# Optimization experiments

Hardware: AMD Instinct MI355X
Metric: run time of the kernel (lower is better)

Reference implementation:

```python
import jax, jax.numpy as jnp
import numpy as np

N_NODES = 50000


def setup_inputs() -> dict:
    key = jax.random.key(0)
    k1, k2, k3, k4, k5 = jax.random.split(key, 5)
    h = jax.random.normal(k1, (50000, 256), dtype=jnp.float32)
    norm = jax.random.uniform(k2, (50000, 1), dtype=jnp.float32)
    weight = jax.random.normal(k3, (256, 96), dtype=jnp.float32) * (1.0 / np.sqrt(96.0))
    src = jax.random.randint(k4, (800000,), 0, N_NODES, dtype=jnp.int64)
    dst = jax.random.randint(k5, (800000,), 0, N_NODES, dtype=jnp.int64)
    return {"h": h, "norm": norm, "weight": weight, "src": src, "dst": dst}


def reference(h, norm, weight, src, dst):
    # dense projection: [N, in] @ [in, out] -> [N, out]
    hw = jnp.matmul(h, weight)
    # pre-aggregation degree norm
    hw = hw * norm
    # copy_src + sum: gather messages from src, scatter-add into dst
    msgs = hw[src]  # [E, out]
    agg = jax.ops.segment_sum(msgs, dst, num_segments=N_NODES)
    # post-aggregation degree norm + activation
    out = jax.nn.relu(agg * norm)
    return out
```

## Files before the change

kernel.cpp:

```cpp
#include <hip/hip_runtime.h>

#define M_NODES 50000
#define KDIM    256
#define NDIM    96
#define NEDGE   800000
#define BM      64
#define NPB     64
#define NBUCK   782
#define CAPB    1536
#define EPB     2048
#define NBLK_SC 391

typedef short bf16x8 __attribute__((ext_vector_type(8)));
typedef float f32x4  __attribute__((ext_vector_type(4)));

__device__ inline unsigned short f2bf(float x) {
    unsigned u = __float_as_uint(x);
    u = (u + 0x7fffu + ((u >> 16) & 1u)) >> 16;
    return (unsigned short)u;
}
__device__ inline unsigned pack2bf(float x, float y) {
    return (unsigned)f2bf(x) | ((unsigned)f2bf(y) << 16);
}

__global__ __launch_bounds__(256) void prep_w_kernel(
    const float* __restrict__ w, unsigned short* __restrict__ wt,
    int* __restrict__ gcursor)
{
    if (blockIdx.x == 0)
        for (int i = threadIdx.x; i < NBUCK; i += 256)
            gcursor[i] = i * CAPB;
    int i = blockIdx.x * 256 + threadIdx.x;
    if (i < KDIM * NDIM) {
        int n = i >> 8;
        int k = i & 255;
        wt[i] = f2bf(w[(size_t)k * NDIM + n]);
    }
}

__global__ __launch_bounds__(256) void gemm_mfma_kernel(
    const float* __restrict__ h, const float* __restrict__ norm,
    const unsigned short* __restrict__ wt, unsigned short* __restrict__ hwb)
{
    __shared__ unsigned short w_lds[96 * 256];

    const int tid  = threadIdx.x;
    const int lane = tid & 63;
    const int wv   = tid >> 6;
    const int row0 = blockIdx.x * BM;

#pragma unroll
    for (int it = 0; it < 12; ++it) {
        int idx = tid + it * 256;
        int n   = idx >> 5;
        int kb  = (idx & 31) * 16;
        uint4 v = *reinterpret_cast<const uint4*>(
            reinterpret_cast<const char*>(wt) + n * 512 + kb);
        *reinterpret_cast<uint4*>(
            reinterpret_cast<char*>(w_lds) + n * 512 + (kb ^ ((n & 7) << 4))) = v;
    }
    __syncthreads();

    f32x4 acc[6];
#pragma unroll
    for (int f = 0; f < 6; ++f) acc[f] = (f32x4){0.f, 0.f, 0.f, 0.f};

    const int ar  = wv * 16 + (lane & 15);
    const int kg  = lane >> 4;
    int arow = row0 + ar;
    if (arow >= M_NODES) arow = M_NODES - 1;
    const float* __restrict__ hrow = h + (size_t)arow * KDIM;

#pragma unroll
    for (int s = 0; s < 8; ++s) {
        const int k0 = s * 32 + kg * 8;
        float4 p = *reinterpret_cast<const float4*>(hrow + k0);
        float4 q = *reinterpret_cast<const float4*>(hrow + k0 + 4);
        union { bf16x8 v; unsigned u[4]; } a;
        a.u[0] = pack2bf(p.x, p.y);
        a.u[1] = pack2bf(p.z, p.w);
        a.u[2] = pack2bf(q.x, q.y);
        a.u[3] = pack2bf(q.z, q.w);

        const int kb = s * 64 + kg * 16;
#pragma unroll
        for (int f = 0; f < 6; ++f) {
            int n = f * 16 + (lane & 15);
            bf16x8 b = *reinterpret_cast<const bf16x8*>(
                reinterpret_cast<const char*>(w_lds) + n * 512 + (kb ^ ((n & 7) << 4)));
            acc[f] = __builtin_amdgcn_mfma_f32_16x16x32_bf16(a.v, b, acc[f], 0, 0, 0);
        }
    }

    const int crow = wv * 16 + (lane >> 4) * 4;
    const int ccol = lane & 15;
#pragma unroll
    for (int r = 0; r < 4; ++r) {
        int row = row0 + crow + r;
        if (row < M_NODES) {
            float nv = norm[row];
#pragma unroll
            for (int f = 0; f < 6; ++f)
                hwb[(size_t)row * NDIM + f * 16 + ccol] = f2bf(acc[f][r] * nv);
        }
    }
}

__global__ __launch_bounds__(256) void bin_scatter_kernel(
    const int* __restrict__ src, const int* __restrict__ dst,
    int* __restrict__ gcursor, unsigned* __restrict__ binned)
{
    __shared__ int cnt[NBUCK];
    __shared__ int base[NBUCK];
    const int t  = threadIdx.x;
    const int e0 = blockIdx.x * EPB;
    const int e1 = (e0 + EPB < NEDGE) ? e0 + EPB : NEDGE;

    for (int i = t; i < NBUCK; i += 256) cnt[i] = 0;
    __syncthreads();
    for (int e = e0 + t; e < e1; e += 256)
        atomicAdd(&cnt[dst[e] >> 6], 1);
    __syncthreads();
    for (int i = t; i < NBUCK; i += 256) {
        int c = cnt[i];
        base[i] = c ? atomicAdd(&gcursor[i], c) : 0;
    }
    __syncthreads();
    for (int i = t; i < NBUCK; i += 256) cnt[i] = 0;
    __syncthreads();
    for (int e = e0 + t; e < e1; e += 256) {
        int d = dst[e];
        int b = d >> 6;
        int pos = base[b] + atomicAdd(&cnt[b], 1);
        if (pos < (b + 1) * CAPB)
            binned[pos] = ((unsigned)(d & 63) << 16) | (unsigned)src[e];
    }
}

#define ACC8(v)                                        \
    acc[0] += __uint_as_float((v).x << 16);            \
    acc[1] += __uint_as_float((v).x & 0xffff0000u);    \
    acc[2] += __uint_as_float((v).y << 16);            \
    acc[3] += __uint_as_float((v).y & 0xffff0000u);    \
    acc[4] += __uint_as_float((v).z << 16);            \
    acc[5] += __uint_as_float((v).z & 0xffff0000u);    \
    acc[6] += __uint_as_float((v).w << 16);            \
    acc[7] += __uint_as_float((v).w & 0xffff0000u);

__global__ __launch_bounds__(256) void csr_agg_kernel(
    const unsigned* __restrict__ binned, const int* __restrict__ gcursor,
    const unsigned short* __restrict__ hwb, const float* __restrict__ norm,
    float* __restrict__ out)
{
    __shared__ unsigned eL[CAPB];
    __shared__ unsigned short oL[CAPB];
    __shared__ int cnt[NPB];
    __shared__ int pfxE[NPB];

    const int b  = blockIdx.x;
    const int t  = threadIdx.x;
    const int e0 = b * CAPB;
    int cntE = gcursor[b] - e0;
    if (cntE > CAPB) cntE = CAPB;

    for (int i = t; i < cntE; i += 256) eL[i] = binned[e0 + i];
    if (t < NPB) cnt[t] = 0;
    __syncthreads();
    for (int i = t; i < cntE; i += 256)
        atomicAdd(&cnt[(eL[i] >> 16) & 63], 1);
    __syncthreads();
    if (t < NPB) pfxE[t] = cnt[t];
    __syncthreads();
    for (int st = 1; st < NPB; st <<= 1) {
        int o = (t >= st && t < NPB) ? pfxE[t - st] : 0;
        __syncthreads();
        if (t < NPB) pfxE[t] += o;
        __syncthreads();
    }
    if (t < NPB) {
        int ex = pfxE[t] - cnt[t];
        pfxE[t] = ex;
        cnt[t]  = ex;
    }
    __syncthreads();
    for (int i = t; i < cntE; i += 256) {
        unsigned v = eL[i];
        int d = (v >> 16) & 63;
        int p = atomicAdd(&cnt[d], 1);
        oL[p] = (unsigned short)(v & 0xffffu);
    }
    __syncthreads();

#pragma unroll
    for (int pass = 0; pass < 3; ++pass) {
        const int u     = pass * 256 + t;
        const int node  = u / 12;
        const int c8    = u - node * 12;
        const int gnode = b * NPB + node;
        if (gnode < M_NODES) {
            const int s0 = pfxE[node];
            const int s1 = cnt[node];
            float acc[8] = {0.f, 0.f, 0.f, 0.f, 0.f, 0.f, 0.f, 0.f};
            int e = s0;
            for (; e + 2 <= s1; e += 2) {
                int a0 = oL[e], a1 = oL[e + 1];
                uint4 v0 = *reinterpret_cast<const uint4*>(hwb + (size_t)a0 * NDIM + c8 * 8);
                uint4 v1 = *reinterpret_cast<const uint4*>(hwb + (size_t)a1 * NDIM + c8 * 8);
                ACC8(v0); ACC8(v1);
            }
            if (e < s1) {
                int a0 = oL[e];
                uint4 v0 = *reinterpret_cast<const uint4*>(hwb + (size_t)a0 * NDIM + c8 * 8);
                ACC8(v0);
            }
            const float nv = norm[gnode];
            float4 o0, o1;
            o0.x = fmaxf(acc[0] * nv, 0.f); o0.y = fmaxf(acc[1] * nv, 0.f);
            o0.z = fmaxf(acc[2] * nv, 0.f); o0.w = fmaxf(acc[3] * nv, 0.f);
            o1.x = fmaxf(acc[4] * nv, 0.f); o1.y = fmaxf(acc[5] * nv, 0.f);
            o1.z = fmaxf(acc[6] * nv, 0.f); o1.w = fmaxf(acc[7] * nv, 0.f);
            float4* po = reinterpret_cast<float4*>(out + (size_t)gnode * NDIM + c8 * 8);
            po[0] = o0; po[1] = o1;
        }
    }
}

extern "C" void kernel_launch(void* const* d_in, const int* in_sizes, int n_in,
                              void* d_out, int out_size, void* d_ws, size_t ws_size,
                              hipStream_t stream)
{
    const float* h    = (const float*)d_in[0];
    const float* norm = (const float*)d_in[1];
    const float* w    = (const float*)d_in[2];
    const int*   src  = (const int*)d_in[3];
    const int*   dst  = (const int*)d_in[4];
    float* out = (float*)d_out;

    unsigned short* hwb = (unsigned short*)d_ws;
    unsigned short* wt  = hwb + (size_t)M_NODES * NDIM;
    int* gcursor = (int*)(wt + KDIM * NDIM);
    unsigned* binned = (unsigned*)(gcursor + 800);

    prep_w_kernel<<<(KDIM * NDIM + 255) / 256, 256, 0, stream>>>(w, wt, gcursor);
    bin_scatter_kernel<<<NBLK_SC, 256, 0, stream>>>(src, dst, gcursor, binned);
    gemm_mfma_kernel<<<(M_NODES + BM - 1) / BM, 256, 0, stream>>>(h, norm, wt, hwb);
    csr_agg_kernel<<<NBUCK, 256, 0, stream>>>(binned, gcursor, hwb, norm, out);
}
```

Measured before the change: 75.89 us.

## Merge GEMM and edge binning into one launch, double GEMM rows per block

```diff
diff --git a/kernel.cpp b/kernel.cpp
--- a/kernel.cpp
+++ b/kernel.cpp
@@ -4,7 +4,8 @@
 #define KDIM    256
 #define NDIM    96
 #define NEDGE   800000
-#define BM      64
+#define BM      128
+#define GEMM_BLKS 391
 #define NPB     64
 #define NBUCK   782
 #define CAPB    1536
@@ -38,114 +39,131 @@
     }
 }
 
-__global__ __launch_bounds__(256) void gemm_mfma_kernel(
+__global__ __launch_bounds__(256) void fused_gemm_scatter_kernel(
     const float* __restrict__ h, const float* __restrict__ norm,
-    const unsigned short* __restrict__ wt, unsigned short* __restrict__ hwb)
-{
-    __shared__ unsigned short w_lds[96 * 256];
-
-    const int tid  = threadIdx.x;
-    const int lane = tid & 63;
-    const int wv   = tid >> 6;
-    const int row0 = blockIdx.x * BM;
-
-#pragma unroll
-    for (int it = 0; it < 12; ++it) {
-        int idx = tid + it * 256;
-        int n   = idx >> 5;
-        int kb  = (idx & 31) * 16;
-        uint4 v = *reinterpret_cast<const uint4*>(
-            reinterpret_cast<const char*>(wt) + n * 512 + kb);
-        *reinterpret_cast<uint4*>(
-            reinterpret_cast<char*>(w_lds) + n * 512 + (kb ^ ((n & 7) << 4))) = v;
-    }
-    __syncthreads();
-
-    f32x4 acc[6];
-#pragma unroll
-    for (int f = 0; f < 6; ++f) acc[f] = (f32x4){0.f, 0.f, 0.f, 0.f};
-
-    const int ar  = wv * 16 + (lane & 15);
-    const int kg  = lane >> 4;
-    int arow = row0 + ar;
-    if (arow >= M_NODES) arow = M_NODES - 1;
-    const float* __restrict__ hrow = h + (size_t)arow * KDIM;
-
-#pragma unroll
-    for (int s = 0; s < 8; ++s) {
-        const int k0 = s * 32 + kg * 8;
-        float4 p = *reinterpret_cast<const float4*>(hrow + k0);
-        float4 q = *reinterpret_cast<const float4*>(hrow + k0 + 4);
-        union { bf16x8 v; unsigned u[4]; } a;
-        a.u[0] = pack2bf(p.x, p.y);
-        a.u[1] = pack2bf(p.z, p.w);
-        a.u[2] = pack2bf(q.x, q.y);
-        a.u[3] = pack2bf(q.z, q.w);
-
-        const int kb = s * 64 + kg * 16;
-#pragma unroll
-        for (int f = 0; f < 6; ++f) {
-            int n = f * 16 + (lane & 15);
-            bf16x8 b = *reinterpret_cast<const bf16x8*>(
-                reinterpret_cast<const char*>(w_lds) + n * 512 + (kb ^ ((n & 7) << 4)));
-            acc[f] = __builtin_amdgcn_mfma_f32_16x16x32_bf16(a.v, b, acc[f], 0, 0, 0);
-        }
-    }
-
-    const int crow = wv * 16 + (lane >> 4) * 4;
-    const int ccol = lane & 15;
-#pragma unroll
-    for (int r = 0; r < 4; ++r) {
-        int row = row0 + crow + r;
-        if (row < M_NODES) {
-            float nv = norm[row];
-#pragma unroll
-            for (int f = 0; f < 6; ++f)
-                hwb[(size_t)row * NDIM + f * 16 + ccol] = f2bf(acc[f][r] * nv);
-        }
-    }
-}
-
-__global__ __launch_bounds__(256) void bin_scatter_kernel(
+    const unsigned short* __restrict__ wt, unsigned short* __restrict__ hwb,
     const int* __restrict__ src, const int* __restrict__ dst,
     int* __restrict__ gcursor, unsigned* __restrict__ binned)
 {
-    __shared__ int cnt[NBUCK];
-    __shared__ int base[NBUCK];
-    const int t  = threadIdx.x;
-    const int e0 = blockIdx.x * EPB;
-    const int e1 = (e0 + EPB < NEDGE) ? e0 + EPB : NEDGE;
-
-    for (int i = t; i < NBUCK; i += 256) cnt[i] = 0;
-    __syncthreads();
-    for (int e = e0 + t; e < e1; e += 256)
-        atomicAdd(&cnt[dst[e] >> 6], 1);
-    __syncthreads();
-    for (int i = t; i < NBUCK; i += 256) {
-        int c = cnt[i];
-        base[i] = c ? atomicAdd(&gcursor[i], c) : 0;
-    }
-    __syncthreads();
-    for (int i = t; i < NBUCK; i += 256) cnt[i] = 0;
-    __syncthreads();
-    for (int e = e0 + t; e < e1; e += 256) {
-        int d = dst[e];
-        int b = d >> 6;
-        int pos = base[b] + atomicAdd(&cnt[b], 1);
-        if (pos < (b + 1) * CAPB)
-            binned[pos] = ((unsigned)(d & 63) << 16) | (unsigned)src[e];
-    }
-}
-
-#define ACC8(v)                                        \
-    acc[0] += __uint_as_float((v).x << 16);            \
-    acc[1] += __uint_as_float((v).x & 0xffff0000u);    \
-    acc[2] += __uint_as_float((v).y << 16);            \
-    acc[3] += __uint_as_float((v).y & 0xffff0000u);    \
-    acc[4] += __uint_as_float((v).z << 16);            \
-    acc[5] += __uint_as_float((v).z & 0xffff0000u);    \
-    acc[6] += __uint_as_float((v).w << 16);            \
-    acc[7] += __uint_as_float((v).w & 0xffff0000u);
+    __shared__ __align__(16) char smem[96 * 512];
+
+    const int tid = threadIdx.x;
+
+    if (blockIdx.x < GEMM_BLKS) {
+        unsigned short* w_lds = reinterpret_cast<unsigned short*>(smem);
+        const int lane = tid & 63;
+        const int wv   = tid >> 6;
+        const int row0 = blockIdx.x * BM;
+
+#pragma unroll
+        for (int it = 0; it < 12; ++it) {
+            int idx = tid + it * 256;
+            int n   = idx >> 5;
+            int kb  = (idx & 31) * 16;
+            uint4 v = *reinterpret_cast<const uint4*>(
+                reinterpret_cast<const char*>(wt) + n * 512 + kb);
+            *reinterpret_cast<uint4*>(
+                reinterpret_cast<char*>(w_lds) + n * 512 + (kb ^ ((n & 7) << 4))) = v;
+        }
+        __syncthreads();
+
+        f32x4 acc0[6], acc1[6];
+#pragma unroll
+        for (int f = 0; f < 6; ++f) {
+            acc0[f] = (f32x4){0.f, 0.f, 0.f, 0.f};
+            acc1[f] = (f32x4){0.f, 0.f, 0.f, 0.f};
+        }
+
+        const int ar = wv * 16 + (lane & 15);
+        const int kg = lane >> 4;
+        int arow0 = row0 + ar;
+        int arow1 = row0 + ar + 64;
+        if (arow0 >= M_NODES) arow0 = M_NODES - 1;
+        if (arow1 >= M_NODES) arow1 = M_NODES - 1;
+        const float* __restrict__ hr0 = h + (size_t)arow0 * KDIM;
+        const float* __restrict__ hr1 = h + (size_t)arow1 * KDIM;
+
+#pragma unroll
+        for (int s = 0; s < 8; ++s) {
+            const int k0 = s * 32 + kg * 8;
+            float4 p0 = *reinterpret_cast<const float4*>(hr0 + k0);
+            float4 q0 = *reinterpret_cast<const float4*>(hr0 + k0 + 4);
+            float4 p1 = *reinterpret_cast<const float4*>(hr1 + k0);
+            float4 q1 = *reinterpret_cast<const float4*>(hr1 + k0 + 4);
+            union { bf16x8 v; unsigned u[4]; } a0, a1;
+            a0.u[0] = pack2bf(p0.x, p0.y); a0.u[1] = pack2bf(p0.z, p0.w);
+            a0.u[2] = pack2bf(q0.x, q0.y); a0.u[3] = pack2bf(q0.z, q0.w);
+            a1.u[0] = pack2bf(p1.x, p1.y); a1.u[1] = pack2bf(p1.z, p1.w);
+            a1.u[2] = pack2bf(q1.x, q1.y); a1.u[3] = pack2bf(q1.z, q1.w);
+
+            const int kb = s * 64 + kg * 16;
+#pragma unroll
+            for (int f = 0; f < 6; ++f) {
+                int n = f * 16 + (lane & 15);
+                bf16x8 b = *reinterpret_cast<const bf16x8*>(
+                    reinterpret_cast<const char*>(w_lds) + n * 512 + (kb ^ ((n & 7) << 4)));
+                acc0[f] = __builtin_amdgcn_mfma_f32_16x16x32_bf16(a0.v, b, acc0[f], 0, 0, 0);
+                acc1[f] = __builtin_amdgcn_mfma_f32_16x16x32_bf16(a1.v, b, acc1[f], 0, 0, 0);
+            }
+        }
+
+        const int crow = wv * 16 + (lane >> 4) * 4;
+        const int ccol = lane & 15;
+#pragma unroll
+        for (int r = 0; r < 4; ++r) {
+            int rowA = row0 + crow + r;
+            if (rowA < M_NODES) {
+                float nv = norm[rowA];
+#pragma unroll
+                for (int f = 0; f < 6; ++f)
+                    hwb[(size_t)rowA * NDIM + f * 16 + ccol] = f2bf(acc0[f][r] * nv);
+            }
+            int rowB = rowA + 64;
+            if (rowB < M_NODES) {
+                float nv = norm[rowB];
+#pragma unroll
+                for (int f = 0; f < 6; ++f)
+                    hwb[(size_t)rowB * NDIM + f * 16 + ccol] = f2bf(acc1[f][r] * nv);
+            }
+        }
+    } else {
+        int* cnt  = reinterpret_cast<int*>(smem);
+        int* base = cnt + NBUCK;
+        const int blk = blockIdx.x - GEMM_BLKS;
+        const int e0 = blk * EPB;
+        const int e1 = (e0 + EPB < NEDGE) ? e0 + EPB : NEDGE;
+
+        for (int i = tid; i < NBUCK; i += 256) cnt[i] = 0;
+        __syncthreads();
+        for (int e = e0 + tid; e < e1; e += 256)
+            atomicAdd(&cnt[dst[e] >> 6], 1);
+        __syncthreads();
+        for (int i = tid; i < NBUCK; i += 256) {
+            int c = cnt[i];
+            base[i] = c ? atomicAdd(&gcursor[i], c) : 0;
+        }
+        __syncthreads();
+        for (int i = tid; i < NBUCK; i += 256) cnt[i] = 0;
+        __syncthreads();
+        for (int e = e0 + tid; e < e1; e += 256) {
+            int d = dst[e];
+            int b = d >> 6;
+            int pos = base[b] + atomicAdd(&cnt[b], 1);
+            if (pos < (b + 1) * CAPB)
+                binned[pos] = ((unsigned)(d & 63) << 16) | (unsigned)src[e];
+        }
+    }
+}
+
+#define ACCV(A, v)                                     \
+    A[0] += __uint_as_float((v).x << 16);              \
+    A[1] += __uint_as_float((v).x & 0xffff0000u);      \
+    A[2] += __uint_as_float((v).y << 16);              \
+    A[3] += __uint_as_float((v).y & 0xffff0000u);      \
+    A[4] += __uint_as_float((v).z << 16);              \
+    A[5] += __uint_as_float((v).z & 0xffff0000u);      \
+    A[6] += __uint_as_float((v).w << 16);              \
+    A[7] += __uint_as_float((v).w & 0xffff0000u);
 
 __global__ __launch_bounds__(256) void csr_agg_kernel(
     const unsigned* __restrict__ binned, const int* __restrict__ gcursor,
@@ -200,25 +218,32 @@
         if (gnode < M_NODES) {
             const int s0 = pfxE[node];
             const int s1 = cnt[node];
-            float acc[8] = {0.f, 0.f, 0.f, 0.f, 0.f, 0.f, 0.f, 0.f};
+            float acc[8]  = {0.f, 0.f, 0.f, 0.f, 0.f, 0.f, 0.f, 0.f};
+            float acc2[8] = {0.f, 0.f, 0.f, 0.f, 0.f, 0.f, 0.f, 0.f};
             int e = s0;
-            for (; e + 2 <= s1; e += 2) {
-                int a0 = oL[e], a1 = oL[e + 1];
+            for (; e + 4 <= s1; e += 4) {
+                int a0 = oL[e], a1 = oL[e + 1], a2 = oL[e + 2], a3 = oL[e + 3];
                 uint4 v0 = *reinterpret_cast<const uint4*>(hwb + (size_t)a0 * NDIM + c8 * 8);
                 uint4 v1 = *reinterpret_cast<const uint4*>(hwb + (size_t)a1 * NDIM + c8 * 8);
-                ACC8(v0); ACC8(v1);
-            }
-            if (e < s1) {
+                uint4 v2 = *reinterpret_cast<const uint4*>(hwb + (size_t)a2 * NDIM + c8 * 8);
+                uint4 v3 = *reinterpret_cast<const uint4*>(hwb + (size_t)a3 * NDIM + c8 * 8);
+                ACCV(acc, v0); ACCV(acc2, v1); ACCV(acc, v2); ACCV(acc2, v3);
+            }
+            for (; e < s1; ++e) {
                 int a0 = oL[e];
                 uint4 v0 = *reinterpret_cast<const uint4*>(hwb + (size_t)a0 * NDIM + c8 * 8);
-                ACC8(v0);
+                ACCV(acc, v0);
             }
             const float nv = norm[gnode];
             float4 o0, o1;
-            o0.x = fmaxf(acc[0] * nv, 0.f); o0.y = fmaxf(acc[1] * nv, 0.f);
-            o0.z = fmaxf(acc[2] * nv, 0.f); o0.w = fmaxf(acc[3] * nv, 0.f);
-            o1.x = fmaxf(acc[4] * nv, 0.f); o1.y = fmaxf(acc[5] * nv, 0.f);
-            o1.z = fmaxf(acc[6] * nv, 0.f); o1.w = fmaxf(acc[7] * nv, 0.f);
+            o0.x = fmaxf((acc[0] + acc2[0]) * nv, 0.f);
+            o0.y = fmaxf((acc[1] + acc2[1]) * nv, 0.f);
+            o0.z = fmaxf((acc[2] + acc2[2]) * nv, 0.f);
+            o0.w = fmaxf((acc[3] + acc2[3]) * nv, 0.f);
+            o1.x = fmaxf((acc[4] + acc2[4]) * nv, 0.f);
+            o1.y = fmaxf((acc[5] + acc2[5]) * nv, 0.f);
+            o1.z = fmaxf((acc[6] + acc2[6]) * nv, 0.f);
+            o1.w = fmaxf((acc[7] + acc2[7]) * nv, 0.f);
             float4* po = reinterpret_cast<float4*>(out + (size_t)gnode * NDIM + c8 * 8);
             po[0] = o0; po[1] = o1;
         }
@@ -242,7 +267,7 @@
     unsigned* binned = (unsigned*)(gcursor + 800);
 
     prep_w_kernel<<<(KDIM * NDIM + 255) / 256, 256, 0, stream>>>(w, wt, gcursor);
-    bin_scatter_kernel<<<NBLK_SC, 256, 0, stream>>>(src, dst, gcursor, binned);
-    gemm_mfma_kernel<<<(M_NODES + BM - 1) / BM, 256, 0, stream>>>(h, norm, wt, hwb);
+    fused_gemm_scatter_kernel<<<GEMM_BLKS + NBLK_SC, 256, 0, stream>>>(
+        h, norm, wt, hwb, src, dst, gcursor, binned);
     csr_agg_kernel<<<NBUCK, 256, 0, stream>>>(binned, gcursor, hwb, norm, out);
 }
```

Result: faster. 70.36 us (-7.3%).
